# Optimization experiments

Hardware: AMD Instinct MI355X
Metric: run time of the kernel (lower is better)

Reference implementation:

```python
import jax, jax.numpy as jnp
import numpy as np

B, N, E, L = 64, 50000, 1600000, 20
BN_EPS = 1e-5


def setup_inputs() -> dict:
    key = jax.random.key(0)
    ks = jax.random.split(key, 8)
    x = jax.random.normal(ks[0], (B, N), dtype=jnp.float32)
    edge_index = jax.random.randint(ks[1], (2, E), 0, N, dtype=jnp.int32)
    alpha = jax.random.normal(ks[2], (E,), dtype=jnp.float32)
    bias = jax.random.normal(ks[3], (E,), dtype=jnp.float32)
    # LazyLinear(num_labels) on [B, N] features
    W = jax.random.normal(ks[4], (L, N), dtype=jnp.float32) / np.sqrt(N)
    b_lin = jax.random.normal(ks[5], (L,), dtype=jnp.float32) * 0.01
    # LazyBatchNorm1d affine params over N features
    gamma = jnp.ones((N,), dtype=jnp.float32)
    beta = jnp.zeros((N,), dtype=jnp.float32)
    return {"x": x, "edge_index": edge_index, "alpha": alpha, "bias": bias,
            "W": W, "b_lin": b_lin, "gamma": gamma, "beta": beta}


def reference(x, edge_index, alpha, bias, W, b_lin, gamma, beta):
    src, dst = edge_index[0], edge_index[1]
    # gather per-edge source features and apply per-edge affine: [B, E]
    x_e = alpha * x[:, src] + bias
    # scatter-mean into destination nodes: [B, N]
    sums = jnp.zeros((x.shape[0], N), dtype=x.dtype).at[:, dst].add(x_e)
    counts = jnp.zeros((N,), dtype=x.dtype).at[dst].add(1.0)
    x_hat = sums / jnp.maximum(counts, 1.0)
    out = jnp.tanh(x_hat)
    # linear head: [B, L]
    pred = x_hat @ W.T + b_lin
    # BatchNorm1d (training mode: batch stats, biased variance)
    mu = jnp.mean(out, axis=0)
    var = jnp.var(out, axis=0)
    bn = (out - mu) / jnp.sqrt(var + BN_EPS) * gamma + beta
    return (pred, bn)
```

## Files before the change

kernel.cpp:

```cpp
#include <hip/hip_runtime.h>
#include <math.h>

#define NB 64
#define NL 20
#define BN_EPS 1e-5f

#define BIN_W 64
#define NBIN 782
#define NBINP 1024
#define BIN_CAP 2560
#define CHUNK 2048

__device__ __forceinline__ unsigned short f2bf(float f) {
    unsigned u = __float_as_uint(f);
    unsigned r = u + 0x7fff + ((u >> 16) & 1);
    return (unsigned short)(r >> 16);
}
__device__ __forceinline__ float bf2f(unsigned short h) {
    return __uint_as_float(((unsigned)h) << 16);
}

__global__ __launch_bounds__(256) void transpose_kernel(
    const float* __restrict__ x, unsigned short* __restrict__ xTb, int Nn) {
    __shared__ float tile[64][65];
    int n0 = blockIdx.x * 64;
    int ln = threadIdx.x & 63;
    int wv = threadIdx.x >> 6;
    for (int r = wv; r < 64; r += 4) {
        int col = n0 + ln;
        tile[r][ln] = (col < Nn) ? x[r * Nn + col] : 0.f;
    }
    __syncthreads();
    for (int r = wv; r < 64; r += 4) {
        int node = n0 + r;
        if (node < Nn) xTb[(size_t)node * 64 + ln] = f2bf(tile[ln][r]);
    }
}

__global__ __launch_bounds__(1024) void binsort_kernel(
    const int* __restrict__ src, const int* __restrict__ dst,
    const float* __restrict__ alpha, const float* __restrict__ bias,
    int* __restrict__ cursor, uint2* __restrict__ paybins, int E) {
    __shared__ unsigned hist[NBINP];
    __shared__ unsigned scn[NBINP];
    __shared__ unsigned gbase[NBINP];
    __shared__ unsigned wsum[16];
    __shared__ uint2 ord[CHUNK];

    int tid = threadIdx.x;
    int e0 = blockIdx.x * CHUNK;

    hist[tid] = 0;
    __syncthreads();

    uint2 pay[2];
    unsigned rk[2];
    int bn[2];
    #pragma unroll
    for (int k = 0; k < 2; ++k) {
        int e = e0 + k * 1024 + tid;
        bn[k] = -1;
        if (e < E) {
            int d = dst[e];
            int b = d >> 6;
            int dl = d & 63;
            pay[k].x = (unsigned)src[e] | ((unsigned)f2bf(alpha[e]) << 16);
            pay[k].y = (unsigned)f2bf(bias[e]) | ((unsigned)dl << 16) |
                       ((unsigned)b << 22);
            bn[k] = b;
            rk[k] = atomicAdd(&hist[b], 1u);
        }
    }
    __syncthreads();

    unsigned v = hist[tid];
    unsigned incl = v;
    #pragma unroll
    for (int off = 1; off < 64; off <<= 1) {
        unsigned t = __shfl_up(incl, off, 64);
        if ((tid & 63) >= off) incl += t;
    }
    if ((tid & 63) == 63) wsum[tid >> 6] = incl;
    __syncthreads();
    if (tid < 16) {
        unsigned y = wsum[tid];
        unsigned yi = y;
        #pragma unroll
        for (int off = 1; off < 16; off <<= 1) {
            unsigned t = __shfl_up(yi, off, 64);
            if (tid >= off) yi += t;
        }
        wsum[tid] = yi - y;
    }
    __syncthreads();
    unsigned excl = incl - v + wsum[tid >> 6];
    scn[tid] = excl;
    if (v > 0) gbase[tid] = atomicAdd(&cursor[tid], (int)v);
    __syncthreads();

    #pragma unroll
    for (int k = 0; k < 2; ++k)
        if (bn[k] >= 0) ord[scn[bn[k]] + rk[k]] = pay[k];
    __syncthreads();

    int cc = E - e0;
    if (cc > CHUNK) cc = CHUNK;
    for (int p = tid; p < cc; p += 1024) {
        uint2 w = ord[p];
        unsigned b = w.y >> 22;
        unsigned di = gbase[b] + ((unsigned)p - scn[b]);
        if (di < BIN_CAP)
            paybins[(size_t)b * BIN_CAP + di] = w;
    }
}

__global__ __launch_bounds__(512) void pull_fin2_kernel(
    const int* __restrict__ cursor, const uint2* __restrict__ paybins,
    const unsigned short* __restrict__ xTb, const float* __restrict__ W,
    const float* __restrict__ gamma, const float* __restrict__ beta,
    float* __restrict__ pred_part, float* __restrict__ bn, int Nn) {
    __shared__ __align__(16) char smem[33280];
    uint2*          ed    = (uint2*)smem;
    unsigned short* order = (unsigned short*)(smem + BIN_CAP * 8);
    float (*xh)[65] = (float (*)[65])smem;
    float (*th)[65] = (float (*)[65])(smem + 16640);

    __shared__ float wl[NL][64];
    __shared__ unsigned h2[64], b2[64], c2[64];
    __shared__ float mu_s[64], a_s[64], be_s[64];

    int bin = blockIdx.x;
    int tid = threadIdx.x;
    int ln = tid & 63;
    int w = tid >> 6;
    int n0 = bin * 64;

    int cnt = cursor[bin];
    if (cnt > BIN_CAP) cnt = BIN_CAP;

    for (int i = tid; i < NL * 64; i += 512) {
        int l = i >> 6, j = i & 63;
        wl[l][j] = (n0 + j < Nn) ? W[l * Nn + n0 + j] : 0.f;
    }
    for (int i = tid; i < cnt; i += 512)
        ed[i] = paybins[(size_t)bin * BIN_CAP + i];
    if (tid < 64) { h2[tid] = 0; c2[tid] = 0; }
    __syncthreads();

    for (int i = tid; i < cnt; i += 512)
        atomicAdd(&h2[(ed[i].y >> 16) & 63], 1u);
    __syncthreads();

    if (tid < 64) {
        unsigned v = h2[tid];
        unsigned incl = v;
        #pragma unroll
        for (int off = 1; off < 64; off <<= 1) {
            unsigned t = __shfl_up(incl, off, 64);
            if (tid >= off) incl += t;
        }
        b2[tid] = incl - v;
    }
    __syncthreads();

    for (int i = tid; i < cnt; i += 512) {
        unsigned dl = (ed[i].y >> 16) & 63;
        unsigned r = atomicAdd(&c2[dl], 1u);
        order[b2[dl] + r] = (unsigned short)i;
    }
    __syncthreads();

    float xh_reg[8], th_reg[8];
    #pragma unroll
    for (int k = 0; k < 8; ++k) {
        int dl = w * 8 + k;
        int node = n0 + dl;
        int n = (int)h2[dl];
        unsigned bs = b2[dl];
        float acc0 = 0.f, acc1 = 0.f, bsum = 0.f;
        int j = 0;
        for (; j + 1 < n; j += 2) {
            unsigned i0 = order[bs + j];
            unsigned i1 = order[bs + j + 1];
            uint2 w0 = ed[i0];
            uint2 w1 = ed[i1];
            float a0 = __uint_as_float(w0.x & 0xffff0000u);
            float a1 = __uint_as_float(w1.x & 0xffff0000u);
            bsum += __uint_as_float((w0.y & 0xffffu) << 16) +
                    __uint_as_float((w1.y & 0xffffu) << 16);
            acc0 = fmaf(a0, bf2f(xTb[(size_t)(w0.x & 0xffffu) * 64 + ln]), acc0);
            acc1 = fmaf(a1, bf2f(xTb[(size_t)(w1.x & 0xffffu) * 64 + ln]), acc1);
        }
        if (j < n) {
            unsigned i0 = order[bs + j];
            uint2 w0 = ed[i0];
            float a0 = __uint_as_float(w0.x & 0xffff0000u);
            bsum += __uint_as_float((w0.y & 0xffffu) << 16);
            acc0 = fmaf(a0, bf2f(xTb[(size_t)(w0.x & 0xffffu) * 64 + ln]), acc0);
        }
        float xhat = 0.f;
        if (node < Nn)
            xhat = (acc0 + acc1 + bsum) / fmaxf((float)n, 1.0f);
        xh_reg[k] = xhat;
        th_reg[k] = tanhf(xhat);
    }
    __syncthreads();

    #pragma unroll
    for (int k = 0; k < 8; ++k) {
        xh[w * 8 + k][ln] = xh_reg[k];
        th[w * 8 + k][ln] = th_reg[k];
    }
    __syncthreads();

    {
        float acc[3] = {0.f, 0.f, 0.f};
        for (int n = 0; n < 64; ++n) {
            float xv = xh[n][ln];
            #pragma unroll
            for (int k = 0; k < 3; ++k) {
                int l = w + k * 8;
                if (l < NL) acc[k] = fmaf(xv, wl[l][n], acc[k]);
            }
        }
        #pragma unroll
        for (int k = 0; k < 3; ++k) {
            int l = w + k * 8;
            if (l < NL)
                pred_part[(size_t)bin * (NB * NL) + ln * NL + l] = acc[k];
        }
    }

    if (tid < 64) {
        int node = n0 + tid;
        float sum = 0.f, sq = 0.f;
        for (int bb = 0; bb < 64; ++bb) {
            float v = th[tid][bb];
            sum += v;
            sq = fmaf(v, v, sq);
        }
        float mu = sum * (1.0f / 64.0f);
        float var = fmaxf(sq * (1.0f / 64.0f) - mu * mu, 0.f);
        float inv = rsqrtf(var + BN_EPS);
        float gm = 1.f, bt = 0.f;
        if (node < Nn) { gm = gamma[node]; bt = beta[node]; }
        mu_s[tid] = mu;
        a_s[tid] = inv * gm;
        be_s[tid] = bt;
    }
    __syncthreads();

    for (int idx = tid; idx < 64 * 64; idx += 512) {
        int noff = idx & 63, bb = idx >> 6;
        int node = n0 + noff;
        if (node < Nn)
            bn[bb * Nn + node] =
                fmaf(th[noff][bb] - mu_s[noff], a_s[noff], be_s[noff]);
    }
}

__global__ __launch_bounds__(256) void reduce_pred_kernel(
    const float* __restrict__ part, const float* __restrict__ b_lin,
    float* __restrict__ pred, int nblk) {
    int out = blockIdx.x * 4 + (threadIdx.x >> 6);
    if (out >= NB * NL) return;
    int ln = threadIdx.x & 63;
    float s = 0.f;
    for (int i = ln; i < nblk; i += 64)
        s += part[(size_t)i * (NB * NL) + out];
    #pragma unroll
    for (int off = 32; off > 0; off >>= 1)
        s += __shfl_xor(s, off, 64);
    if (ln == 0) pred[out] = b_lin[out % NL] + s;
}

extern "C" void kernel_launch(void* const* d_in, const int* in_sizes, int n_in,
                              void* d_out, int out_size, void* d_ws, size_t ws_size,
                              hipStream_t stream) {
    const float* x     = (const float*)d_in[0];
    const int*   ei    = (const int*)d_in[1];
    const float* alpha = (const float*)d_in[2];
    const float* bias  = (const float*)d_in[3];
    const float* W     = (const float*)d_in[4];
    const float* b_lin = (const float*)d_in[5];
    const float* gamma = (const float*)d_in[6];
    const float* beta  = (const float*)d_in[7];

    const int Nn = in_sizes[0] / NB;
    const int E  = in_sizes[1] / 2;
    const int* src = ei;
    const int* dst = ei + E;

    const int ntile = (Nn + 63) / 64;

    uint2*          paybins = (uint2*)d_ws;
    unsigned short* xTb     = (unsigned short*)(paybins + (size_t)NBIN * BIN_CAP);
    int*            cursor  = (int*)(xTb + (size_t)Nn * 64);
    float*          pred_part = (float*)(cursor + NBIN);

    float* pred = (float*)d_out;
    float* bn   = pred + NB * NL;

    hipMemsetAsync(cursor, 0, NBIN * sizeof(int), stream);

    transpose_kernel<<<ntile, 256, 0, stream>>>(x, xTb, Nn);
    binsort_kernel<<<(E + CHUNK - 1) / CHUNK, 1024, 0, stream>>>(
        src, dst, alpha, bias, cursor, paybins, E);
    pull_fin2_kernel<<<NBIN, 512, 0, stream>>>(cursor, paybins, xTb, W,
                                               gamma, beta, pred_part, bn, Nn);
    reduce_pred_kernel<<<(NB * NL + 3) / 4, 256, 0, stream>>>(
        pred_part, b_lin, pred, NBIN);
}
```

Before: 213.4 us.

## Sort edge payloads directly in LDS, unroll gather by four, fuse BN stats via shuffles

The pull kernel now keeps each thread's payloads in registers and scatters them into LDS already sorted by destination node. This removes the separate index array and the double-indirect lookup. The gather loop is unrolled by four with independent accumulators for more memory-level parallelism. BatchNorm statistics are computed with wave shuffles inside the gather loop, which removes a serial 64-thread pass and a barrier. The binsort chunk also doubles to 4096 edges per block, so fewer global cursor atomics are needed at the cost of more registers. The myp[5] buffer is correct only while no more than 2560 edges fall in a bin, which matches BIN_CAP.

```diff
diff --git a/kernel.cpp b/kernel.cpp
--- a/kernel.cpp
+++ b/kernel.cpp
@@ -9,7 +9,7 @@
 #define NBIN 782
 #define NBINP 1024
 #define BIN_CAP 2560
-#define CHUNK 2048
+#define CHUNK 4096
 
 __device__ __forceinline__ unsigned short f2bf(float f) {
     unsigned u = __float_as_uint(f);
@@ -53,11 +53,11 @@
     hist[tid] = 0;
     __syncthreads();
 
-    uint2 pay[2];
-    unsigned rk[2];
-    int bn[2];
-    #pragma unroll
-    for (int k = 0; k < 2; ++k) {
+    uint2 pay[4];
+    unsigned rk[4];
+    int bn[4];
+    #pragma unroll
+    for (int k = 0; k < 4; ++k) {
         int e = e0 + k * 1024 + tid;
         bn[k] = -1;
         if (e < E) {
@@ -99,7 +99,7 @@
     __syncthreads();
 
     #pragma unroll
-    for (int k = 0; k < 2; ++k)
+    for (int k = 0; k < 4; ++k)
         if (bn[k] >= 0) ord[scn[bn[k]] + rk[k]] = pay[k];
     __syncthreads();
 
@@ -120,8 +120,7 @@
     const float* __restrict__ gamma, const float* __restrict__ beta,
     float* __restrict__ pred_part, float* __restrict__ bn, int Nn) {
     __shared__ __align__(16) char smem[33280];
-    uint2*          ed    = (uint2*)smem;
-    unsigned short* order = (unsigned short*)(smem + BIN_CAP * 8);
+    uint2* ed = (uint2*)smem;
     float (*xh)[65] = (float (*)[65])smem;
     float (*th)[65] = (float (*)[65])(smem + 16640);
 
@@ -137,18 +136,22 @@
 
     int cnt = cursor[bin];
     if (cnt > BIN_CAP) cnt = BIN_CAP;
+    const uint2* pb = paybins + (size_t)bin * BIN_CAP;
 
     for (int i = tid; i < NL * 64; i += 512) {
         int l = i >> 6, j = i & 63;
         wl[l][j] = (n0 + j < Nn) ? W[l * Nn + n0 + j] : 0.f;
     }
-    for (int i = tid; i < cnt; i += 512)
-        ed[i] = paybins[(size_t)bin * BIN_CAP + i];
     if (tid < 64) { h2[tid] = 0; c2[tid] = 0; }
     __syncthreads();
 
-    for (int i = tid; i < cnt; i += 512)
-        atomicAdd(&h2[(ed[i].y >> 16) & 63], 1u);
+    uint2 myp[5];
+    int nm = 0;
+    for (int i = tid; i < cnt; i += 512) {
+        uint2 p = pb[i];
+        myp[nm++] = p;
+        atomicAdd(&h2[(p.y >> 16) & 63], 1u);
+    }
     __syncthreads();
 
     if (tid < 64) {
@@ -163,10 +166,10 @@
     }
     __syncthreads();
 
-    for (int i = tid; i < cnt; i += 512) {
-        unsigned dl = (ed[i].y >> 16) & 63;
+    for (int k = 0; k < nm; ++k) {
+        unsigned dl = (myp[k].y >> 16) & 63;
         unsigned r = atomicAdd(&c2[dl], 1u);
-        order[b2[dl] + r] = (unsigned short)i;
+        ed[b2[dl] + r] = myp[k];
     }
     __syncthreads();
 
@@ -177,32 +180,55 @@
         int node = n0 + dl;
         int n = (int)h2[dl];
         unsigned bs = b2[dl];
-        float acc0 = 0.f, acc1 = 0.f, bsum = 0.f;
+        float a0 = 0.f, a1 = 0.f, a2 = 0.f, a3 = 0.f, bsum = 0.f;
         int j = 0;
-        for (; j + 1 < n; j += 2) {
-            unsigned i0 = order[bs + j];
-            unsigned i1 = order[bs + j + 1];
-            uint2 w0 = ed[i0];
-            uint2 w1 = ed[i1];
-            float a0 = __uint_as_float(w0.x & 0xffff0000u);
-            float a1 = __uint_as_float(w1.x & 0xffff0000u);
-            bsum += __uint_as_float((w0.y & 0xffffu) << 16) +
-                    __uint_as_float((w1.y & 0xffffu) << 16);
-            acc0 = fmaf(a0, bf2f(xTb[(size_t)(w0.x & 0xffffu) * 64 + ln]), acc0);
-            acc1 = fmaf(a1, bf2f(xTb[(size_t)(w1.x & 0xffffu) * 64 + ln]), acc1);
-        }
-        if (j < n) {
-            unsigned i0 = order[bs + j];
-            uint2 w0 = ed[i0];
-            float a0 = __uint_as_float(w0.x & 0xffff0000u);
-            bsum += __uint_as_float((w0.y & 0xffffu) << 16);
-            acc0 = fmaf(a0, bf2f(xTb[(size_t)(w0.x & 0xffffu) * 64 + ln]), acc0);
+        for (; j + 3 < n; j += 4) {
+            uint2 e0 = ed[bs + j];
+            uint2 e1 = ed[bs + j + 1];
+            uint2 e2 = ed[bs + j + 2];
+            uint2 e3 = ed[bs + j + 3];
+            bsum += __uint_as_float((e0.y & 0xffffu) << 16) +
+                    __uint_as_float((e1.y & 0xffffu) << 16) +
+                    __uint_as_float((e2.y & 0xffffu) << 16) +
+                    __uint_as_float((e3.y & 0xffffu) << 16);
+            a0 = fmaf(__uint_as_float(e0.x & 0xffff0000u),
+                      bf2f(xTb[(size_t)(e0.x & 0xffffu) * 64 + ln]), a0);
+            a1 = fmaf(__uint_as_float(e1.x & 0xffff0000u),
+                      bf2f(xTb[(size_t)(e1.x & 0xffffu) * 64 + ln]), a1);
+            a2 = fmaf(__uint_as_float(e2.x & 0xffff0000u),
+                      bf2f(xTb[(size_t)(e2.x & 0xffffu) * 64 + ln]), a2);
+            a3 = fmaf(__uint_as_float(e3.x & 0xffff0000u),
+                      bf2f(xTb[(size_t)(e3.x & 0xffffu) * 64 + ln]), a3);
+        }
+        for (; j < n; ++j) {
+            uint2 e0 = ed[bs + j];
+            bsum += __uint_as_float((e0.y & 0xffffu) << 16);
+            a0 = fmaf(__uint_as_float(e0.x & 0xffff0000u),
+                      bf2f(xTb[(size_t)(e0.x & 0xffffu) * 64 + ln]), a0);
         }
         float xhat = 0.f;
         if (node < Nn)
-            xhat = (acc0 + acc1 + bsum) / fmaxf((float)n, 1.0f);
+            xhat = ((a0 + a1) + (a2 + a3) + bsum) / fmaxf((float)n, 1.0f);
         xh_reg[k] = xhat;
-        th_reg[k] = tanhf(xhat);
+        float tv = tanhf(xhat);
+        th_reg[k] = tv;
+
+        float s = tv, q = tv * tv;
+        #pragma unroll
+        for (int off = 32; off > 0; off >>= 1) {
+            s += __shfl_xor(s, off, 64);
+            q += __shfl_xor(q, off, 64);
+        }
+        if (ln == 0) {
+            float mu = s * (1.0f / 64.0f);
+            float var = fmaxf(q * (1.0f / 64.0f) - mu * mu, 0.f);
+            float inv = rsqrtf(var + BN_EPS);
+            float gm = 1.f, bt = 0.f;
+            if (node < Nn) { gm = gamma[node]; bt = beta[node]; }
+            mu_s[dl] = mu;
+            a_s[dl] = inv * gm;
+            be_s[dl] = bt;
+        }
     }
     __syncthreads();
 
@@ -230,25 +256,6 @@
                 pred_part[(size_t)bin * (NB * NL) + ln * NL + l] = acc[k];
         }
     }
-
-    if (tid < 64) {
-        int node = n0 + tid;
-        float sum = 0.f, sq = 0.f;
-        for (int bb = 0; bb < 64; ++bb) {
-            float v = th[tid][bb];
-            sum += v;
-            sq = fmaf(v, v, sq);
-        }
-        float mu = sum * (1.0f / 64.0f);
-        float var = fmaxf(sq * (1.0f / 64.0f) - mu * mu, 0.f);
-        float inv = rsqrtf(var + BN_EPS);
-        float gm = 1.f, bt = 0.f;
-        if (node < Nn) { gm = gamma[node]; bt = beta[node]; }
-        mu_s[tid] = mu;
-        a_s[tid] = inv * gm;
-        be_s[tid] = bt;
-    }
-    __syncthreads();
 
     for (int idx = tid; idx < 64 * 64; idx += 512) {
         int noff = idx & 63, bb = idx >> 6;
```

Result: no change. 212.3 us (-0.5%).
